# Kernel tuning notes

Measured on AMD Instinct MI355X. Metric: run time of the kernel, lower is better.

The kernel has to match this reference:

```python
import jax, jax.numpy as jnp
import numpy as np

HID = 5120       # hidden_size
H = 32           # num_heads (TP shard)
Q_RANK = 1536    # q_lora_rank
KV_RANK = 512    # kv_lora_rank
D_NOPE = 128     # qk_nope_head_dim
D_ROPE = 64      # qk_rope_head_dim
DV = 128         # v_head_dim
Q_HEAD = D_NOPE + D_ROPE
T = 2048
EPS = 1e-6
ROPE_BASE = 10000.0
SCALE = Q_HEAD ** -0.5
NEG = jnp.finfo(jnp.float32).min


def rmsnorm(x, w):
    return x * jax.lax.rsqrt(jnp.mean(x * x, axis=-1, keepdims=True) + EPS) * w


def rope(x, pos):
    # half-split (GPT-NeoX style) rotary; the torch module permutes weights in
    # _update_pe so that interleaved RoPE becomes exactly this half-split form.
    half = x.shape[-1] // 2
    inv = 1.0 / (ROPE_BASE ** (jnp.arange(half, dtype=jnp.float32) / half))
    ang = pos.astype(jnp.float32)[:, None] * inv          # [T, half]
    cos, sin = jnp.cos(ang), jnp.sin(ang)
    if x.ndim == 3:                                       # [T, H, D]
        cos, sin = cos[:, None, :], sin[:, None, :]
    x1, x2 = jnp.split(x, 2, axis=-1)
    return jnp.concatenate([x1 * cos - x2 * sin, x2 * cos + x1 * sin], axis=-1)


def setup_inputs() -> dict:
    key = jax.random.key(0)
    ks = jax.random.split(key, 10)
    s = 0.02
    return {
        'hidden_states': jax.random.normal(ks[0], (1, T, HID), jnp.float32),
        'position_ids': jnp.arange(T, dtype=jnp.int64),
        'w_q_a': jax.random.normal(ks[1], (Q_RANK, HID), jnp.float32) * s,
        'q_a_ln_w': jnp.ones((Q_RANK,), jnp.float32),
        'w_q_b': jax.random.normal(ks[2], (H * Q_HEAD, Q_RANK), jnp.float32) * s,
        'w_kv_a': jax.random.normal(ks[3], (KV_RANK + D_ROPE, HID), jnp.float32) * s,
        'kv_a_ln_w': jnp.ones((KV_RANK,), jnp.float32),
        'w_kc': jax.random.normal(ks[4], (H, D_NOPE, KV_RANK), jnp.float32) * s,
        'w_vc': jax.random.normal(ks[5], (H, KV_RANK, DV), jnp.float32) * s,
        'w_o': jax.random.normal(ks[6], (HID, H * DV), jnp.float32) * s,
    }


def reference(hidden_states, position_ids, w_q_a, q_a_ln_w, w_q_b, w_kv_a,
              kv_a_ln_w, w_kc, w_vc, w_o):
    h = hidden_states[0]                                   # [T, HID]
    t = h.shape[0]
    # q low-rank path: q_a_proj -> rmsnorm -> q_b_proj
    q = rmsnorm(h @ w_q_a.T, q_a_ln_w) @ w_q_b.T           # [T, H*Q_HEAD]
    q = q.reshape(t, H, Q_HEAD)
    q_nope, q_pe = q[..., :D_NOPE], q[..., D_NOPE:]
    # absorb kv_b (w_kc): project q into the latent kv space
    q_lat = jnp.einsum('thn,hnk->thk', q_nope, w_kc)       # [T, H, KV_RANK]
    # kv low-rank path (MQA-style shared latent)
    ckv_full = h @ w_kv_a.T                                # [T, KV_RANK+D_ROPE]
    ckv = rmsnorm(ckv_full[:, :KV_RANK], kv_a_ln_w)        # [T, KV_RANK]
    k_pe = rope(ckv_full[:, KV_RANK:], position_ids)       # [T, D_ROPE]
    q_pe = rope(q_pe, position_ids)                        # [T, H, D_ROPE]
    # full query/key in latent+pe space; key/value shared across heads
    qf = jnp.concatenate([q_lat, q_pe], axis=-1)           # [T, H, KV_RANK+D_ROPE]
    kf = jnp.concatenate([ckv, k_pe], axis=-1)             # [T, KV_RANK+D_ROPE]
    scores = jnp.einsum('thd,sd->hts', qf, kf) * SCALE     # [H, T, T]
    causal = jnp.tril(jnp.ones((t, t), dtype=bool))
    scores = jnp.where(causal[None], scores, NEG)
    p = jax.nn.softmax(scores, axis=-1)
    o = jnp.einsum('hts,sk->thk', p, ckv)                  # [T, H, KV_RANK]
    o = jnp.einsum('thk,hkv->thv', o, w_vc)                # [T, H, DV]
    out = o.reshape(t, H * DV) @ w_o.T                     # [T, HID]
    return out[None]
```

## Files before the change

### kernel.cpp

```cpp
#include <hip/hip_runtime.h>
#include <hip/hip_bf16.h>
#include <type_traits>

typedef __attribute__((ext_vector_type(8))) short short8;
typedef __attribute__((ext_vector_type(4))) float f32x4;
using bf16 = __hip_bfloat16;

#define T_SEQ 2048
#define NH 32
#define SCALE_F 0.07216878364870323f

__device__ inline unsigned short f2bf(float f) {
    unsigned u = __builtin_bit_cast(unsigned, f);
    return (unsigned short)((u + 0x7fffu + ((u >> 16) & 1u)) >> 16);
}

__device__ inline void gload_lds16(const void* g, void* l) {
    __builtin_amdgcn_global_load_lds(
        (const __attribute__((address_space(1))) unsigned*)g,
        (__attribute__((address_space(3))) unsigned*)l, 16, 0, 0);
}

__device__ inline int sw4(int r) { return (r & 3) ^ ((r >> 2) & 3); }

template <typename TC>
__global__ __launch_bounds__(512, 4) void gemm256_kernel(
    const bf16* __restrict__ A, const bf16* __restrict__ B, TC* __restrict__ C,
    int K, int lda, int ldb, int ldc,
    long aStride, long bStride, long cStride)
{
    const int z = blockIdx.z;
    A += (long)z * aStride; B += (long)z * bStride; C += (long)z * cStride;
    const int bm = blockIdx.y * 256, bn = blockIdx.x * 128;
    __shared__ __align__(16) short As[2][256 * 32];
    __shared__ __align__(16) short Bs[2][128 * 32];
    const int tid = threadIdx.x, lane = tid & 63, w = tid >> 6;
    const int l15 = lane & 15, lg = lane >> 4;
    const int wm = w >> 1, wn = w & 1;
    const int lr = lane >> 2;
    const int lcol = ((lane & 3) ^ sw4(lr)) * 8;
    const int arow0 = 32 * w + lr, arow1 = 32 * w + 16 + lr;
    const int brow = 16 * w + lr;
    const bf16* Ab = A + (long)bm * lda;
    const bf16* Bb = B + (long)bn * ldb;

    auto stage = [&](int buf, int k0) {
        gload_lds16(Ab + (long)arow0 * lda + k0 + lcol, &As[buf][(2 * w) * 512]);
        gload_lds16(Ab + (long)arow1 * lda + k0 + lcol, &As[buf][(2 * w + 1) * 512]);
        gload_lds16(Bb + (long)brow * ldb + k0 + lcol, &Bs[buf][w * 512]);
    };

    const int rs = sw4(l15);
    f32x4 acc[4][4] = {};
    const int nt = K >> 5;
    stage(0, 0);
    for (int t = 0; t < nt; ++t) {
        if (t + 1 < nt) {
            stage((t + 1) & 1, (t + 1) << 5);
            asm volatile("s_waitcnt vmcnt(3)" ::: "memory");
        } else {
            asm volatile("s_waitcnt vmcnt(0)" ::: "memory");
        }
        __builtin_amdgcn_s_barrier();
        __builtin_amdgcn_sched_barrier(0);
        const char* Ap = (const char*)&As[t & 1][0];
        const char* Bp = (const char*)&Bs[t & 1][0];
        short8 af[4], bf[4];
        #pragma unroll
        for (int fi = 0; fi < 4; ++fi)
            af[fi] = *(const short8*)(Ap + (wm * 64 + fi * 16 + l15) * 64
                                      + ((lg ^ rs) << 4));
        #pragma unroll
        for (int nj = 0; nj < 4; ++nj)
            bf[nj] = *(const short8*)(Bp + (wn * 64 + nj * 16 + l15) * 64
                                      + ((lg ^ rs) << 4));
        #pragma unroll
        for (int fi = 0; fi < 4; ++fi)
            #pragma unroll
            for (int nj = 0; nj < 4; ++nj)
                acc[fi][nj] = __builtin_amdgcn_mfma_f32_16x16x32_bf16(
                    af[fi], bf[nj], acc[fi][nj], 0, 0, 0);
        asm volatile("s_waitcnt lgkmcnt(0)" ::: "memory");
        __builtin_amdgcn_sched_barrier(0);
        __builtin_amdgcn_s_barrier();
        __builtin_amdgcn_sched_barrier(0);
    }
    #pragma unroll
    for (int fi = 0; fi < 4; ++fi)
        #pragma unroll
        for (int nj = 0; nj < 4; ++nj)
            #pragma unroll
            for (int i = 0; i < 4; ++i) {
                const int row = bm + wm * 64 + fi * 16 + lg * 4 + i;
                const int col = bn + wn * 64 + nj * 16 + l15;
                if constexpr (std::is_same<TC, float>::value)
                    C[(long)row * ldc + col] = acc[fi][nj][i];
                else
                    ((unsigned short*)C)[(long)row * ldc + col] = f2bf(acc[fi][nj][i]);
            }
}

template <typename TC>
__global__ __launch_bounds__(512, 4) void gemm8w_kernel(
    const bf16* __restrict__ A, const bf16* __restrict__ B, TC* __restrict__ C,
    int K, int lda, int ldb, int ldc,
    long aStride, long bStride, long cStride)
{
    const int z = blockIdx.z;
    A += (long)z * aStride; B += (long)z * bStride; C += (long)z * cStride;
    const int bm = blockIdx.y * 128, bn = blockIdx.x * 128;
    __shared__ __align__(16) short As[2][128 * 64];
    __shared__ __align__(16) short Bs[2][128 * 64];
    const int tid = threadIdx.x, lane = tid & 63, w = tid >> 6;
    const int l15 = lane & 15, lg = lane >> 4;
    const int wm = w >> 1, wn = w & 1;
    const int c0 = w * 2, c1 = w * 2 + 1;
    const int srow0 = c0 * 8 + (lane >> 3), srow1 = c1 * 8 + (lane >> 3);
    const int scol = ((lane & 7) * 16) ^ ((lane >> 3) << 4);
    const bf16* Ab = A + (long)bm * lda;
    const bf16* Bb = B + (long)bn * ldb;

    auto stage = [&](int buf, int k0) {
        const char* ag = (const char*)(Ab + k0);
        const char* bg = (const char*)(Bb + k0);
        gload_lds16(ag + (long)srow0 * (lda * 2) + scol, &As[buf][c0 * 512]);
        gload_lds16(ag + (long)srow1 * (lda * 2) + scol, &As[buf][c1 * 512]);
        gload_lds16(bg + (long)srow0 * (ldb * 2) + scol, &Bs[buf][c0 * 512]);
        gload_lds16(bg + (long)srow1 * (ldb * 2) + scol, &Bs[buf][c1 * 512]);
    };

    const int swz = (l15 & 7) << 4;
    f32x4 acc[2][4] = {};
    const int nt = K >> 6;
    stage(0, 0);
    for (int t = 0; t < nt; ++t) {
        if (t + 1 < nt) {
            stage((t + 1) & 1, (t + 1) << 6);
            asm volatile("s_waitcnt vmcnt(4)" ::: "memory");
        } else {
            asm volatile("s_waitcnt vmcnt(0)" ::: "memory");
        }
        __builtin_amdgcn_s_barrier();
        __builtin_amdgcn_sched_barrier(0);
        const char* Ap = (const char*)&As[t & 1][0];
        const char* Bp = (const char*)&Bs[t & 1][0];
        short8 af[2][2], bfv[4][2];
        #pragma unroll
        for (int fi = 0; fi < 2; ++fi)
            #pragma unroll
            for (int ks = 0; ks < 2; ++ks)
                af[fi][ks] = *(const short8*)(Ap + (wm * 32 + fi * 16 + l15) * 128
                                              + ((ks * 64 + lg * 16) ^ swz));
        #pragma unroll
        for (int nj = 0; nj < 4; ++nj)
            #pragma unroll
            for (int ks = 0; ks < 2; ++ks)
                bfv[nj][ks] = *(const short8*)(Bp + (wn * 64 + nj * 16 + l15) * 128
                                               + ((ks * 64 + lg * 16) ^ swz));
        #pragma unroll
        for (int ks = 0; ks < 2; ++ks)
            #pragma unroll
            for (int fi = 0; fi < 2; ++fi)
                #pragma unroll
                for (int nj = 0; nj < 4; ++nj)
                    acc[fi][nj] = __builtin_amdgcn_mfma_f32_16x16x32_bf16(
                        af[fi][ks], bfv[nj][ks], acc[fi][nj], 0, 0, 0);
        asm volatile("s_waitcnt lgkmcnt(0)" ::: "memory");
        __builtin_amdgcn_sched_barrier(0);
        __builtin_amdgcn_s_barrier();
        __builtin_amdgcn_sched_barrier(0);
    }
    #pragma unroll
    for (int fi = 0; fi < 2; ++fi)
        #pragma unroll
        for (int nj = 0; nj < 4; ++nj)
            #pragma unroll
            for (int i = 0; i < 4; ++i) {
                const int row = bm + wm * 32 + fi * 16 + lg * 4 + i;
                const int col = bn + wn * 64 + nj * 16 + l15;
                if constexpr (std::is_same<TC, float>::value)
                    C[(long)row * ldc + col] = acc[fi][nj][i];
                else
                    ((unsigned short*)C)[(long)row * ldc + col] = f2bf(acc[fi][nj][i]);
            }
}

__global__ __launch_bounds__(256) void cvt_kernel(
    const float* __restrict__ in, bf16* __restrict__ out, long n, float scale)
{
    const long i = ((long)blockIdx.x * 256 + threadIdx.x) * 8;
    if (i >= n) return;
    f32x4 a = *(const f32x4*)(in + i), b = *(const f32x4*)(in + i + 4);
    short8 r;
    r[0] = (short)f2bf(a[0] * scale); r[1] = (short)f2bf(a[1] * scale);
    r[2] = (short)f2bf(a[2] * scale); r[3] = (short)f2bf(a[3] * scale);
    r[4] = (short)f2bf(b[0] * scale); r[5] = (short)f2bf(b[1] * scale);
    r[6] = (short)f2bf(b[2] * scale); r[7] = (short)f2bf(b[3] * scale);
    *(short8*)(out + i) = r;
}

__global__ __launch_bounds__(256) void tconv_kernel(
    const float* __restrict__ in, bf16* __restrict__ out)
{
    const int h = blockIdx.z, k0 = blockIdx.x * 32, d0 = blockIdx.y * 32;
    __shared__ float t[32][33];
    const int r = threadIdx.x >> 5, c = threadIdx.x & 31;
    const float* ip = in + ((long)h * 512 + k0) * 128 + d0;
    #pragma unroll
    for (int it = 0; it < 4; ++it)
        t[r + 8 * it][c] = ip[(long)(r + 8 * it) * 128 + c];
    __syncthreads();
    bf16* op = out + ((long)h * 128 + d0) * 512 + k0;
    #pragma unroll
    for (int it = 0; it < 4; ++it)
        op[(long)(r + 8 * it) * 512 + c] = __float2bfloat16(t[c][r + 8 * it]);
}

__global__ __launch_bounds__(256) void rmsnorm_kernel(
    bf16* __restrict__ x, const float* __restrict__ w, int C, int ld)
{
    bf16* row = x + (long)blockIdx.x * ld;
    float ss = 0.f;
    for (int i = threadIdx.x; i < C; i += 256) {
        float v = __bfloat162float(row[i]);
        ss += v * v;
    }
    #pragma unroll
    for (int m = 1; m < 64; m <<= 1) ss += __shfl_xor(ss, m, 64);
    __shared__ float red[4];
    if ((threadIdx.x & 63) == 0) red[threadIdx.x >> 6] = ss;
    __syncthreads();
    ss = red[0] + red[1] + red[2] + red[3];
    float scale = rsqrtf(ss / (float)C + 1e-6f);
    for (int i = threadIdx.x; i < C; i += 256) {
        float v = __bfloat162float(row[i]);
        row[i] = __float2bfloat16(v * scale * w[i]);
    }
}

__global__ __launch_bounds__(256) void ropeq_kernel(bf16* __restrict__ q)
{
    const int t = blockIdx.x;
    #pragma unroll
    for (int it = 0; it < 4; ++it) {
        const int pair = threadIdx.x + 256 * it;
        const int h = pair >> 5, i = pair & 31;
        bf16* base = q + ((long)t * NH + h) * 192;
        float x1 = __bfloat162float(base[128 + i]);
        float x2 = __bfloat162float(base[160 + i]);
        float inv = powf(10000.f, -(float)i / 32.f);
        float ang = (float)t * inv, s, c;
        sincosf(ang, &s, &c);
        base[128 + i] = __float2bfloat16(x1 * c - x2 * s);
        base[160 + i] = __float2bfloat16(x2 * c + x1 * s);
    }
}

__global__ __launch_bounds__(1024) void ropek_kernel(
    const bf16* __restrict__ ckv, bf16* __restrict__ kf, int ld)
{
    const int t = blockIdx.x;
    const int h = threadIdx.x >> 5, i = threadIdx.x & 31;
    float x1 = __bfloat162float(ckv[(long)t * ld + 512 + i]);
    float x2 = __bfloat162float(ckv[(long)t * ld + 544 + i]);
    float inv = powf(10000.f, -(float)i / 32.f);
    float ang = (float)t * inv, s, c;
    sincosf(ang, &s, &c);
    bf16* kb = kf + ((long)h * T_SEQ + t) * 192;
    kb[128 + i] = __float2bfloat16(x1 * c - x2 * s);
    kb[160 + i] = __float2bfloat16(x2 * c + x1 * s);
}

__global__ __launch_bounds__(256, 2) void attn_kernel(
    const bf16* __restrict__ Q,
    const bf16* __restrict__ Kf,
    const bf16* __restrict__ Vt,
    bf16* __restrict__ O)
{
    const int lin = blockIdx.x;
    const int h = (lin & 7) + 8 * ((lin >> 3) & 3);
    const int qraw = lin >> 5;
    const int qblk = (qraw < 8) ? (2 * qraw) : (31 - 2 * qraw);
    const int q0 = qblk * 128;
    const int tid = threadIdx.x, lane = tid & 63, w = tid >> 6;
    const int l15 = lane & 15, lg = lane >> 4;
    const int qw = q0 + w * 32;
    __shared__ __align__(16) short Ks[64 * 192];
    __shared__ __align__(16) short Vs[128 * 64];

    int ksoff[6];
    #pragma unroll
    for (int j = 0; j < 6; ++j) {
        int o = (w * 6 + j) * 1024 + lane * 16;
        int row = o / 384, col = o % 384;
        ksoff[j] = row * 384 + (col ^ ((row & 7) << 4));
    }
    const int vrow8 = lane >> 3;
    const int vscol = ((lane & 7) * 16) ^ (vrow8 << 4);

    short8 qf[2][6];
    #pragma unroll
    for (int qi = 0; qi < 2; ++qi) {
        const bf16* qp = Q + (long)(qw + qi * 16 + l15) * (NH * 192) + (long)h * 192;
        #pragma unroll
        for (int c = 0; c < 6; ++c) qf[qi][c] = *(const short8*)(qp + c * 32 + lg * 8);
    }

    f32x4 oacc[2][8] = {};
    float mst[2] = {-INFINITY, -INFINITY};
    float lst[2] = {0.f, 0.f};

    const char* kbase0 = (const char*)Kf + (long)h * T_SEQ * 384;
    const char* vbase0 = (const char*)Vt + (long)h * 128 * (T_SEQ * 2);
    const int swz = (l15 & 7) << 4;

    for (int s0 = 0; s0 < q0 + 128; s0 += 64) {
        {
            const char* kb = kbase0 + (long)s0 * 384;
            #pragma unroll
            for (int j = 0; j < 6; ++j)
                gload_lds16(kb + ksoff[j], (char*)Ks + (w * 6 + j) * 1024);
            const char* vb = vbase0 + (long)s0 * 2 + vscol;
            #pragma unroll
            for (int j = 0; j < 4; ++j) {
                const int c = w * 4 + j;
                gload_lds16(vb + (long)(c * 8 + vrow8) * (T_SEQ * 2),
                            (char*)Vs + c * 1024);
            }
        }
        __syncthreads();
        if (s0 <= qw + 31) {
            f32x4 st[2][4] = {};
            __builtin_amdgcn_s_setprio(1);
            #pragma unroll
            for (int cb = 0; cb < 4; ++cb) {
                const int krow = cb * 16 + l15;
                #pragma unroll
                for (int c = 0; c < 6; ++c) {
                    short8 kfr = *(const short8*)((const char*)Ks + krow * 384
                                                  + ((c * 64 + lg * 16) ^ swz));
                    st[0][cb] = __builtin_amdgcn_mfma_f32_16x16x32_bf16(kfr, qf[0][c], st[0][cb], 0, 0, 0);
                    st[1][cb] = __builtin_amdgcn_mfma_f32_16x16x32_bf16(kfr, qf[1][c], st[1][cb], 0, 0, 0);
                }
            }
            __builtin_amdgcn_s_setprio(0);
            short8 pb[2][2];
            #pragma unroll
            for (int qi = 0; qi < 2; ++qi) {
                const int qg = qw + qi * 16 + l15;
                float pmax = -INFINITY;
                #pragma unroll
                for (int cb = 0; cb < 4; ++cb)
                    #pragma unroll
                    for (int i = 0; i < 4; ++i) {
                        const int kv = s0 + cb * 16 + lg * 4 + i;
                        float v = (kv <= qg) ? st[qi][cb][i] : -INFINITY;
                        st[qi][cb][i] = v;
                        pmax = fmaxf(pmax, v);
                    }
                pmax = fmaxf(pmax, __shfl_xor(pmax, 16, 64));
                pmax = fmaxf(pmax, __shfl_xor(pmax, 32, 64));
                const float newm = fmaxf(mst[qi], pmax);
                const float mm = (newm == -INFINITY) ? 0.f : newm;
                const float alpha = __expf(mst[qi] - mm);
                float ps = 0.f;
                #pragma unroll
                for (int cb = 0; cb < 4; ++cb)
                    #pragma unroll
                    for (int i = 0; i < 4; ++i) {
                        const float e = __expf(st[qi][cb][i] - mm);
                        st[qi][cb][i] = e; ps += e;
                    }
                ps += __shfl_xor(ps, 16, 64);
                ps += __shfl_xor(ps, 32, 64);
                lst[qi] = lst[qi] * alpha + ps;
                mst[qi] = newm;
                #pragma unroll
                for (int mb = 0; mb < 8; ++mb) oacc[qi][mb] *= alpha;
                #pragma unroll
                for (int hh = 0; hh < 2; ++hh) {
                    unsigned pk[4];
                    #pragma unroll
                    for (int i = 0; i < 4; ++i)
                        pk[i] = (unsigned)f2bf(st[qi][2 * hh][i])
                              | ((unsigned)f2bf(st[qi][2 * hh + 1][i]) << 16);
                    #pragma unroll
                    for (int j = 0; j < 8; ++j) {
                        const int src = l15 + (((2 * lg + (j >> 2)) & 3) << 4);
                        const unsigned u = (unsigned)__shfl((int)pk[j & 3], src, 64);
                        pb[qi][hh][j] = (short)((lg >> 1) ? (u >> 16) : (u & 0xffffu));
                    }
                }
            }
            __builtin_amdgcn_s_setprio(1);
            #pragma unroll
            for (int mb = 0; mb < 8; ++mb) {
                const int vrow = mb * 16 + l15;
                #pragma unroll
                for (int hh = 0; hh < 2; ++hh) {
                    short8 vfr = *(const short8*)((const char*)Vs + vrow * 128
                                                  + ((hh * 64 + lg * 16) ^ swz));
                    oacc[0][mb] = __builtin_amdgcn_mfma_f32_16x16x32_bf16(vfr, pb[0][hh], oacc[0][mb], 0, 0, 0);
                    oacc[1][mb] = __builtin_amdgcn_mfma_f32_16x16x32_bf16(vfr, pb[1][hh], oacc[1][mb], 0, 0, 0);
                }
            }
            __builtin_amdgcn_s_setprio(0);
        }
        __syncthreads();
    }
    #pragma unroll
    for (int qi = 0; qi < 2; ++qi) {
        const float inv = 1.f / lst[qi];
        const int qg = qw + qi * 16 + l15;
        #pragma unroll
        for (int mb = 0; mb < 8; ++mb)
            #pragma unroll
            for (int i = 0; i < 4; ++i) {
                const int dv = mb * 16 + lg * 4 + i;
                O[(long)qg * (NH * 128) + h * 128 + dv] = __float2bfloat16(oacc[qi][mb][i] * inv);
            }
    }
}

extern "C" void kernel_launch(void* const* d_in, const int* in_sizes, int n_in,
                              void* d_out, int out_size, void* d_ws, size_t ws_size,
                              hipStream_t stream)
{
    const float* hidden    = (const float*)d_in[0];
    const float* w_q_a     = (const float*)d_in[2];
    const float* q_a_ln_w  = (const float*)d_in[3];
    const float* w_q_b     = (const float*)d_in[4];
    const float* w_kv_a    = (const float*)d_in[5];
    const float* kv_a_ln_w = (const float*)d_in[6];
    const float* w_kc      = (const float*)d_in[7];
    const float* w_vc      = (const float*)d_in[8];
    const float* w_o       = (const float*)d_in[9];
    float* out = (float*)d_out;

    bf16* qckv  = (bf16*)d_ws;
    bf16* qbuf  = qckv  + (long)T_SEQ * 2176;
    bf16* kf    = qbuf  + (long)T_SEQ * 6144;
    bf16* vt    = kf    + (long)NH * T_SEQ * 192;
    bf16* ov    = vt    + (long)NH * 128 * T_SEQ;
    bf16* hb    = ov    + (long)T_SEQ * 4096;
    bf16* wqckv = hb    + (long)T_SEQ * 5120;
    bf16* wqb   = wqckv + (long)2176 * 5120;
    bf16* wkc   = wqb   + (long)6144 * 1536;
    bf16* wvct  = wkc   + (long)NH * 128 * 512;
    bf16* wo    = hb;
    bf16* ckv   = qckv + 1536;

    cvt_kernel<<<dim3(5120), 256, 0, stream>>>(hidden, hb, (long)T_SEQ * 5120, 1.f);
    cvt_kernel<<<dim3(3840), 256, 0, stream>>>(w_q_a, wqckv, (long)1536 * 5120, 1.f);
    cvt_kernel<<<dim3(1440), 256, 0, stream>>>(w_kv_a, wqckv + (long)1536 * 5120,
                                               (long)576 * 5120, 1.f);
    hipMemsetAsync(wqckv + (long)2112 * 5120, 0, (long)64 * 5120 * sizeof(bf16), stream);
    cvt_kernel<<<dim3(4608), 256, 0, stream>>>(w_q_b, wqb, (long)6144 * 1536, SCALE_F);
    cvt_kernel<<<dim3(1024), 256, 0, stream>>>(w_kc, wkc, (long)NH * 128 * 512, 1.f);
    tconv_kernel<<<dim3(16, 4, NH), 256, 0, stream>>>(w_vc, wvct);

    gemm8w_kernel<bf16><<<dim3(17, 16, 1), 512, 0, stream>>>(
        hb, wqckv, qckv, 5120, 5120, 5120, 2176, 0, 0, 0);
    rmsnorm_kernel<<<dim3(T_SEQ), 256, 0, stream>>>(qckv, q_a_ln_w, 1536, 2176);
    rmsnorm_kernel<<<dim3(T_SEQ), 256, 0, stream>>>(ckv, kv_a_ln_w, 512, 2176);
    gemm256_kernel<bf16><<<dim3(48, 8, 1), 512, 0, stream>>>(
        qckv, wqb, qbuf, 1536, 2176, 1536, 6144, 0, 0, 0);
    ropeq_kernel<<<dim3(T_SEQ), 256, 0, stream>>>(qbuf);
    ropek_kernel<<<dim3(T_SEQ), 1024, 0, stream>>>(ckv, kf, 2176);
    gemm256_kernel<bf16><<<dim3(1, 8, NH), 512, 0, stream>>>(
        ckv, wkc, kf, 512, 2176, 512, 192,
        0, (long)128 * 512, (long)T_SEQ * 192);
    gemm8w_kernel<bf16><<<dim3(16, 1, NH), 512, 0, stream>>>(
        wvct, ckv, vt, 512, 512, 2176, T_SEQ,
        (long)128 * 512, 0, (long)128 * T_SEQ);
    cvt_kernel<<<dim3(10240), 256, 0, stream>>>(w_o, wo, (long)5120 * 4096, 1.f);
    attn_kernel<<<dim3(512), 256, 0, stream>>>(qbuf, kf, vt, ov);
    gemm256_kernel<float><<<dim3(40, 8, 1), 512, 0, stream>>>(
        ov, wo, out, 4096, 4096, 4096, 5120, 0, 0, 0);
}
```

Measured before the change: 486.5 us.

## Halve GEMM workgroup to 4 waves with 128x64 per-wave tiles and new LDS swizzle

The 256x128 GEMM now runs with 256 threads (4 waves) instead of 512, and each wave computes a 128x64 output tile (8x4 MFMA fragments) instead of 64x64. LDS staging and fragment reads use a new XOR swizzle that pairs two rows per 128-byte line. The aim is more register-level reuse per LDS read and less LDS traffic per MFMA. The cost is twice the accumulator registers, fewer waves to hide latency, and a lower occupancy bound (256,2).

Measured after the change: 496.3 us. 1.02x slower.

```diff
diff --git a/kernel.cpp b/kernel.cpp
--- a/kernel.cpp
+++ b/kernel.cpp
@@ -21,10 +21,8 @@
         (__attribute__((address_space(3))) unsigned*)l, 16, 0, 0);
 }
 
-__device__ inline int sw4(int r) { return (r & 3) ^ ((r >> 2) & 3); }
-
 template <typename TC>
-__global__ __launch_bounds__(512, 4) void gemm256_kernel(
+__global__ __launch_bounds__(256, 2) void gemmhw_kernel(
     const bf16* __restrict__ A, const bf16* __restrict__ B, TC* __restrict__ C,
     int K, int lda, int ldb, int ldc,
     long aStride, long bStride, long cStride)
@@ -37,27 +35,37 @@
     const int tid = threadIdx.x, lane = tid & 63, w = tid >> 6;
     const int l15 = lane & 15, lg = lane >> 4;
     const int wm = w >> 1, wn = w & 1;
-    const int lr = lane >> 2;
-    const int lcol = ((lane & 3) ^ sw4(lr)) * 8;
-    const int arow0 = 32 * w + lr, arow1 = 32 * w + 16 + lr;
-    const int brow = 16 * w + lr;
+    const int sx = (lane & 7) ^ (lane >> 3);
+    const int lrh = lane >> 3;
+    const int srp = sx >> 2;
+    const int scol = (sx & 3) * 8;
     const bf16* Ab = A + (long)bm * lda;
     const bf16* Bb = B + (long)bn * ldb;
 
     auto stage = [&](int buf, int k0) {
-        gload_lds16(Ab + (long)arow0 * lda + k0 + lcol, &As[buf][(2 * w) * 512]);
-        gload_lds16(Ab + (long)arow1 * lda + k0 + lcol, &As[buf][(2 * w + 1) * 512]);
-        gload_lds16(Bb + (long)brow * ldb + k0 + lcol, &Bs[buf][w * 512]);
+        #pragma unroll
+        for (int jj = 0; jj < 4; ++jj) {
+            const int j = w * 4 + jj;
+            const int srow = 2 * (j * 8 + lrh) + srp;
+            gload_lds16(Ab + (long)srow * lda + k0 + scol, &As[buf][j * 512]);
+        }
+        #pragma unroll
+        for (int jj = 0; jj < 2; ++jj) {
+            const int j = w * 2 + jj;
+            const int srow = 2 * (j * 8 + lrh) + srp;
+            gload_lds16(Bb + (long)srow * ldb + k0 + scol, &Bs[buf][j * 512]);
+        }
     };
 
-    const int rs = sw4(l15);
-    f32x4 acc[4][4] = {};
+    const int rslot = ((((l15 & 1) << 2) | lg) ^ (l15 >> 1)) << 4;
+    const int lrow_lo = l15 >> 1;
+    f32x4 acc[8][4] = {};
     const int nt = K >> 5;
     stage(0, 0);
     for (int t = 0; t < nt; ++t) {
         if (t + 1 < nt) {
             stage((t + 1) & 1, (t + 1) << 5);
-            asm volatile("s_waitcnt vmcnt(3)" ::: "memory");
+            asm volatile("s_waitcnt vmcnt(6)" ::: "memory");
         } else {
             asm volatile("s_waitcnt vmcnt(0)" ::: "memory");
         }
@@ -65,17 +73,15 @@
         __builtin_amdgcn_sched_barrier(0);
         const char* Ap = (const char*)&As[t & 1][0];
         const char* Bp = (const char*)&Bs[t & 1][0];
-        short8 af[4], bf[4];
-        #pragma unroll
-        for (int fi = 0; fi < 4; ++fi)
-            af[fi] = *(const short8*)(Ap + (wm * 64 + fi * 16 + l15) * 64
-                                      + ((lg ^ rs) << 4));
+        short8 af[8], bf[4];
+        #pragma unroll
+        for (int fi = 0; fi < 8; ++fi)
+            af[fi] = *(const short8*)(Ap + (wm * 64 + fi * 8 + lrow_lo) * 128 + rslot);
         #pragma unroll
         for (int nj = 0; nj < 4; ++nj)
-            bf[nj] = *(const short8*)(Bp + (wn * 64 + nj * 16 + l15) * 64
-                                      + ((lg ^ rs) << 4));
-        #pragma unroll
-        for (int fi = 0; fi < 4; ++fi)
+            bf[nj] = *(const short8*)(Bp + (wn * 32 + nj * 8 + lrow_lo) * 128 + rslot);
+        #pragma unroll
+        for (int fi = 0; fi < 8; ++fi)
             #pragma unroll
             for (int nj = 0; nj < 4; ++nj)
                 acc[fi][nj] = __builtin_amdgcn_mfma_f32_16x16x32_bf16(
@@ -86,12 +92,12 @@
         __builtin_amdgcn_sched_barrier(0);
     }
     #pragma unroll
-    for (int fi = 0; fi < 4; ++fi)
+    for (int fi = 0; fi < 8; ++fi)
         #pragma unroll
         for (int nj = 0; nj < 4; ++nj)
             #pragma unroll
             for (int i = 0; i < 4; ++i) {
-                const int row = bm + wm * 64 + fi * 16 + lg * 4 + i;
+                const int row = bm + wm * 128 + fi * 16 + lg * 4 + i;
                 const int col = bn + wn * 64 + nj * 16 + l15;
                 if constexpr (std::is_same<TC, float>::value)
                     C[(long)row * ldc + col] = acc[fi][nj][i];
@@ -463,11 +469,11 @@
         hb, wqckv, qckv, 5120, 5120, 5120, 2176, 0, 0, 0);
     rmsnorm_kernel<<<dim3(T_SEQ), 256, 0, stream>>>(qckv, q_a_ln_w, 1536, 2176);
     rmsnorm_kernel<<<dim3(T_SEQ), 256, 0, stream>>>(ckv, kv_a_ln_w, 512, 2176);
-    gemm256_kernel<bf16><<<dim3(48, 8, 1), 512, 0, stream>>>(
+    gemmhw_kernel<bf16><<<dim3(48, 8, 1), 256, 0, stream>>>(
         qckv, wqb, qbuf, 1536, 2176, 1536, 6144, 0, 0, 0);
     ropeq_kernel<<<dim3(T_SEQ), 256, 0, stream>>>(qbuf);
     ropek_kernel<<<dim3(T_SEQ), 1024, 0, stream>>>(ckv, kf, 2176);
-    gemm256_kernel<bf16><<<dim3(1, 8, NH), 512, 0, stream>>>(
+    gemmhw_kernel<bf16><<<dim3(1, 8, NH), 256, 0, stream>>>(
         ckv, wkc, kf, 512, 2176, 512, 192,
         0, (long)128 * 512, (long)T_SEQ * 192);
     gemm8w_kernel<bf16><<<dim3(16, 1, NH), 512, 0, stream>>>(
@@ -475,6 +481,6 @@
         (long)128 * 512, 0, (long)128 * T_SEQ);
     cvt_kernel<<<dim3(10240), 256, 0, stream>>>(w_o, wo, (long)5120 * 4096, 1.f);
     attn_kernel<<<dim3(512), 256, 0, stream>>>(qbuf, kf, vt, ov);
-    gemm256_kernel<float><<<dim3(40, 8, 1), 512, 0, stream>>>(
+    gemmhw_kernel<float><<<dim3(40, 8, 1), 256, 0, stream>>>(
         ov, wo, out, 4096, 4096, 4096, 5120, 0, 0, 0);
 }
```
